# Kernel tuning notes

Hardware: AMD Instinct MI355X
Metric: run time of the kernel (lower is better)

## Reference

```python
import jax, jax.numpy as jnp
import numpy as np

N = 100000      # num nodes
E = 1600000     # num edges (avg degree ~16)
D_IN = 64
D_OUT = 64
T = 5.27        # terminal time t
K = 2           # propagation steps


def setup_inputs() -> dict:
    key = jax.random.key(0)
    k1, k2, k3 = jax.random.split(key, 3)
    x = jax.random.normal(k1, (N, D_IN), dtype=jnp.float32)
    edge_index = jax.random.randint(k2, (2, E), 0, N, dtype=jnp.int64)
    # glorot-initialized linear weight [in, out] and bias
    limit = np.sqrt(6.0 / (D_IN + D_OUT)).astype(np.float32)
    W = jax.random.uniform(k3, (D_IN, D_OUT), dtype=jnp.float32, minval=-limit, maxval=limit)
    b = jnp.zeros((D_OUT,), dtype=jnp.float32)
    return {"x": x, "edge_index": edge_index, "W": W, "b": b}


def reference(x, edge_index, W, b):
    n = x.shape[0]
    src, dst = edge_index[0], edge_index[1]
    # add self-loops
    loop = jnp.arange(n, dtype=src.dtype)
    src = jnp.concatenate([src, loop])
    dst = jnp.concatenate([dst, loop])
    w = jnp.ones((src.shape[0],), dtype=x.dtype)
    # symmetric GCN normalization: D^{-1/2} A D^{-1/2}
    deg = jax.ops.segment_sum(w, dst, num_segments=n)
    dinv = jnp.where(deg > 0, jax.lax.rsqrt(deg), jnp.zeros_like(deg))
    w = dinv[src] * w * dinv[dst]
    delta = T / K  # decoupled diffusion step size
    for _ in range(K):
        # spmm: out[i] = sum_{(j->i) in E} w_e * x[j]
        out = jax.ops.segment_sum(x[src] * w[:, None], dst, num_segments=n)
        x = (1.0 - delta) * x + delta * out
    return x @ W + b
```

## Files before the change

### kernel.cpp

```cpp
#include <hip/hip_runtime.h>
#include <hip/hip_fp16.h>


#define TPB 256
#define SCAN_T 256
#define SCAN_I 4
#define SCAN_CHUNK (SCAN_T * SCAN_I)
#define BATCH 16

__global__ void count_kernel(const int* __restrict__ dst, int* __restrict__ counts, int e) {
    int i = blockIdx.x * blockDim.x + threadIdx.x;
    if (i < e) atomicAdd(&counts[dst[i]], 1);
}

__global__ void scan_partials(const int* __restrict__ counts, int* __restrict__ bsums, int n) {
    __shared__ int red[SCAN_T];
    int t = threadIdx.x;
    int base = blockIdx.x * SCAN_CHUNK + t * SCAN_I;
    int s = 0;
#pragma unroll
    for (int k = 0; k < SCAN_I; ++k) { int i = base + k; if (i < n) s += counts[i]; }
    red[t] = s;
    __syncthreads();
    for (int off = SCAN_T / 2; off > 0; off >>= 1) {
        if (t < off) red[t] += red[t + off];
        __syncthreads();
    }
    if (t == 0) bsums[blockIdx.x] = red[0];
}

__global__ void scan_bsums(int* __restrict__ bsums, int nb, int* __restrict__ row_ptr,
                           int n, int e) {
    __shared__ int s[512];
    int t = threadIdx.x;
    int v = (t < nb) ? bsums[t] : 0;
    s[t] = v;
    __syncthreads();
    for (int off = 1; off < 512; off <<= 1) {
        int a = (t >= off) ? s[t - off] : 0;
        __syncthreads();
        s[t] += a;
        __syncthreads();
    }
    if (t < nb) bsums[t] = s[t] - v;
    if (t == 0) row_ptr[n] = e;
}

__global__ void scan_emit(const int* __restrict__ counts, const int* __restrict__ boffs,
                          int* __restrict__ row_ptr, int* __restrict__ cursor,
                          float* __restrict__ dinv, int n) {
    __shared__ int red[SCAN_T];
    int t = threadIdx.x;
    int base = blockIdx.x * SCAN_CHUNK + t * SCAN_I;
    int c[SCAN_I];
    int s = 0;
#pragma unroll
    for (int k = 0; k < SCAN_I; ++k) { int i = base + k; c[k] = (i < n) ? counts[i] : 0; s += c[k]; }
    red[t] = s;
    __syncthreads();
    for (int off = 1; off < SCAN_T; off <<= 1) {
        int a = (t >= off) ? red[t - off] : 0;
        __syncthreads();
        red[t] += a;
        __syncthreads();
    }
    int run = boffs[blockIdx.x] + red[t] - s;
#pragma unroll
    for (int k = 0; k < SCAN_I; ++k) {
        int i = base + k;
        if (i < n) {
            row_ptr[i] = run;
            cursor[i]  = run;
            dinv[i] = rsqrtf((float)(c[k] + 1));
            run += c[k];
        }
    }
}

__global__ void cast_z(const float* __restrict__ x, const float* __restrict__ dinv,
                       __half* __restrict__ zh, __half* __restrict__ z1h, int n) {
    int i = blockIdx.x * blockDim.x + threadIdx.x;
    int total = n * 64;
    if (i < total) {
        zh[i] = __float2half(dinv[i >> 6] * x[i]);
    } else if (i < total + 64) {
        zh[i]  = __float2half(0.f);
        z1h[i] = __float2half(0.f);
    }
}

__global__ void fill_kernel(const int* __restrict__ src, const int* __restrict__ dst,
                            int* __restrict__ cursor, int* __restrict__ col, int e) {
    int i = blockIdx.x * blockDim.x + threadIdx.x;
    if (i >= e) return;
    int pos = atomicAdd(&cursor[dst[i]], 1);
    col[pos] = src[i];
}

__device__ __forceinline__ float spmm_row(const __half* __restrict__ zh,
                                          const int* __restrict__ col,
                                          int beg, int end, int lane, int nzero) {
    float acc = 0.f;
    for (int j = beg; j < end; j += BATCH) {
        int c[BATCH];
#pragma unroll
        for (int k = 0; k < BATCH; ++k) {
            int jj = j + k;
            int cc = col[min(jj, end - 1)];
            c[k] = (jj < end) ? cc : nzero;
        }
        float xv[BATCH];
#pragma unroll
        for (int k = 0; k < BATCH; ++k)
            xv[k] = __half2float(zh[(unsigned)c[k] * 64u + (unsigned)lane]);
#pragma unroll
        for (int k = 0; k < BATCH; ++k) acc += xv[k];
    }
    return acc;
}

__global__ void spmm1_kernel(const float* __restrict__ x, const __half* __restrict__ zh,
                             __half* __restrict__ x1h, __half* __restrict__ z1h,
                             const int* __restrict__ row_ptr, const int* __restrict__ col,
                             const float* __restrict__ dinv, int n, float delta) {
    int node = blockIdx.x * (blockDim.x >> 6) + (threadIdx.x >> 6);
    int lane = threadIdx.x & 63;
    if (node >= n) return;
    unsigned idx = (unsigned)node * 64u + (unsigned)lane;
    float xi = x[idx];
    float dv = dinv[node];
    float acc = spmm_row(zh, col, row_ptr[node], row_ptr[node + 1], lane, n);
    float x1 = (1.f - delta) * xi + delta * dv * (dv * xi + acc);
    x1h[idx] = __float2half(x1);
    z1h[idx] = __float2half(dv * x1);
}

__global__ void spmm2_gemm_kernel(const __half* __restrict__ x1h, const __half* __restrict__ z1h,
                                  float* __restrict__ y,
                                  const int* __restrict__ row_ptr, const int* __restrict__ col,
                                  const float* __restrict__ dinv,
                                  const float* __restrict__ W, const float* __restrict__ b,
                                  int n, float delta) {
    __shared__ float Ws[64 * 64];
    __shared__ float bs[64];
    for (int i = threadIdx.x; i < 64 * 64; i += blockDim.x) Ws[i] = W[i];
    if (threadIdx.x < 64) bs[threadIdx.x] = b[threadIdx.x];
    __syncthreads();
    int node = blockIdx.x * (blockDim.x >> 6) + (threadIdx.x >> 6);
    int lane = threadIdx.x & 63;
    if (node >= n) return;
    unsigned idx = (unsigned)node * 64u + (unsigned)lane;
    float xi = __half2float(x1h[idx]);
    float dv = dinv[node];
    float acc = spmm_row(z1h, col, row_ptr[node], row_ptr[node + 1], lane, n);
    float res = (1.f - delta) * xi + delta * dv * (dv * xi + acc);
    float o = bs[lane];
#pragma unroll
    for (int k = 0; k < 64; ++k) {
        o += __shfl(res, k) * Ws[k * 64 + lane];
    }
    y[idx] = o;
}

extern "C" void kernel_launch(void* const* d_in, const int* in_sizes, int n_in,
                              void* d_out, int out_size, void* d_ws, size_t ws_size,
                              hipStream_t stream) {
    const float* x  = (const float*)d_in[0];
    const int*   ei = (const int*)d_in[1];
    const float* W  = (const float*)d_in[2];
    const float* b  = (const float*)d_in[3];
    float* out = (float*)d_out;

    const int N = in_sizes[0] / 64;
    const int E = in_sizes[1] / 2;
    const float delta = (float)(5.27 / 2.0);

    char* p = (char*)d_ws;
    __half* zh   = (__half*)p;  p += (size_t)(N + 1) * 64 * sizeof(__half);
    __half* z1h  = (__half*)p;  p += (size_t)(N + 1) * 64 * sizeof(__half);
    __half* x1h  = (__half*)p;  p += (size_t)N * 64 * sizeof(__half);
    int*   col   = (int*)p;     p += (size_t)E * sizeof(int);
    float* dinv  = (float*)p;   p += (size_t)N * sizeof(float);
    int*   counts= (int*)p;     p += (size_t)N * sizeof(int);
    int*   rowp  = (int*)p;     p += (size_t)(N + 4) * sizeof(int);
    int*   cursor= (int*)p;     p += (size_t)N * sizeof(int);
    int*   bsums = (int*)p;     p += 512 * sizeof(int);

    hipMemsetAsync(counts, 0, (size_t)N * sizeof(int), stream);

    int grid_e = (E + TPB - 1) / TPB;
    int grid_n = (N + (TPB / 64) - 1) / (TPB / 64);
    int nb_scan = (N + SCAN_CHUNK - 1) / SCAN_CHUNK;
    int grid_c = ((N + 1) * 64 + TPB - 1) / TPB;

    count_kernel<<<grid_e, TPB, 0, stream>>>(ei + E, counts, E);
    scan_partials<<<nb_scan, SCAN_T, 0, stream>>>(counts, bsums, N);
    scan_bsums<<<1, 512, 0, stream>>>(bsums, nb_scan, rowp, N, E);
    scan_emit<<<nb_scan, SCAN_T, 0, stream>>>(counts, bsums, rowp, cursor, dinv, N);
    cast_z<<<grid_c, TPB, 0, stream>>>(x, dinv, zh, z1h, N);
    fill_kernel<<<grid_e, TPB, 0, stream>>>(ei, ei + E, cursor, col, E);

    spmm1_kernel<<<grid_n, TPB, 0, stream>>>(x, zh, x1h, z1h, rowp, col, dinv, N, delta);
    spmm2_gemm_kernel<<<grid_n, TPB, 0, stream>>>(x1h, z1h, out, rowp, col, dinv, W, b, N, delta);
}
```

Baseline: 390.8 us.

## Split wave across two edges with half2 gathers, drop x1h buffer via sqrt-degree recovery

```diff
diff --git a/kernel.cpp b/kernel.cpp
--- a/kernel.cpp
+++ b/kernel.cpp
@@ -48,7 +48,7 @@
 
 __global__ void scan_emit(const int* __restrict__ counts, const int* __restrict__ boffs,
                           int* __restrict__ row_ptr, int* __restrict__ cursor,
-                          float* __restrict__ dinv, int n) {
+                          float* __restrict__ dinv, float* __restrict__ rdeg, int n) {
     __shared__ int red[SCAN_T];
     int t = threadIdx.x;
     int base = blockIdx.x * SCAN_CHUNK + t * SCAN_I;
@@ -71,7 +71,9 @@
         if (i < n) {
             row_ptr[i] = run;
             cursor[i]  = run;
-            dinv[i] = rsqrtf((float)(c[k] + 1));
+            float d = (float)(c[k] + 1);
+            dinv[i] = rsqrtf(d);
+            rdeg[i] = sqrtf(d);
             run += c[k];
         }
     }
@@ -80,12 +82,21 @@
 __global__ void cast_z(const float* __restrict__ x, const float* __restrict__ dinv,
                        __half* __restrict__ zh, __half* __restrict__ z1h, int n) {
     int i = blockIdx.x * blockDim.x + threadIdx.x;
-    int total = n * 64;
+    int total = n * 16;
     if (i < total) {
-        zh[i] = __float2half(dinv[i >> 6] * x[i]);
-    } else if (i < total + 64) {
-        zh[i]  = __float2half(0.f);
-        z1h[i] = __float2half(0.f);
+        float4 v = reinterpret_cast<const float4*>(x)[i];
+        float dv = dinv[i >> 4];
+        __half2 a, b2;
+        a.x  = __float2half(v.x * dv); a.y  = __float2half(v.y * dv);
+        b2.x = __float2half(v.z * dv); b2.y = __float2half(v.w * dv);
+        reinterpret_cast<__half2*>(zh)[2 * i]     = a;
+        reinterpret_cast<__half2*>(zh)[2 * i + 1] = b2;
+    } else if (i < total + 16) {
+        __half2 z; z.x = __float2half(0.f); z.y = __float2half(0.f);
+        reinterpret_cast<__half2*>(zh)[2 * i]      = z;
+        reinterpret_cast<__half2*>(zh)[2 * i + 1]  = z;
+        reinterpret_cast<__half2*>(z1h)[2 * i]     = z;
+        reinterpret_cast<__half2*>(z1h)[2 * i + 1] = z;
     }
 }
 
@@ -97,48 +108,56 @@
     col[pos] = src[i];
 }
 
-__device__ __forceinline__ float spmm_row(const __half* __restrict__ zh,
-                                          const int* __restrict__ col,
-                                          int beg, int end, int lane, int nzero) {
-    float acc = 0.f;
-    for (int j = beg; j < end; j += BATCH) {
+__device__ __forceinline__ float2 spmm_row2(const __half* __restrict__ zh,
+                                            const int* __restrict__ col,
+                                            int beg, int end, int sub, int m, int nzero) {
+    float a0 = 0.f, a1 = 0.f;
+    for (int j = beg; j < end; j += 2 * BATCH) {
         int c[BATCH];
 #pragma unroll
         for (int k = 0; k < BATCH; ++k) {
-            int jj = j + k;
-            int cc = col[min(jj, end - 1)];
-            c[k] = (jj < end) ? cc : nzero;
+            int e = j + 2 * k + sub;
+            int cc = col[min(e, end - 1)];
+            c[k] = (e < end) ? cc : nzero;
         }
-        float xv[BATCH];
+        __half2 v[BATCH];
 #pragma unroll
         for (int k = 0; k < BATCH; ++k)
-            xv[k] = __half2float(zh[(unsigned)c[k] * 64u + (unsigned)lane]);
-#pragma unroll
-        for (int k = 0; k < BATCH; ++k) acc += xv[k];
-    }
-    return acc;
-}
-
-__global__ void spmm1_kernel(const float* __restrict__ x, const __half* __restrict__ zh,
-                             __half* __restrict__ x1h, __half* __restrict__ z1h,
+            v[k] = *reinterpret_cast<const __half2*>(zh + (size_t)(unsigned)c[k] * 64u + 2u * (unsigned)m);
+#pragma unroll
+        for (int k = 0; k < BATCH; ++k) {
+            float2 f = __half22float2(v[k]);
+            a0 += f.x; a1 += f.y;
+        }
+    }
+    a0 += __shfl_xor(a0, 32);
+    a1 += __shfl_xor(a1, 32);
+    return make_float2(a0, a1);
+}
+
+__global__ void spmm1_kernel(const __half* __restrict__ zh, __half* __restrict__ z1h,
                              const int* __restrict__ row_ptr, const int* __restrict__ col,
-                             const float* __restrict__ dinv, int n, float delta) {
+                             const float* __restrict__ dinv, const float* __restrict__ rdeg,
+                             int n, float delta) {
     int node = blockIdx.x * (blockDim.x >> 6) + (threadIdx.x >> 6);
     int lane = threadIdx.x & 63;
     if (node >= n) return;
-    unsigned idx = (unsigned)node * 64u + (unsigned)lane;
-    float xi = x[idx];
-    float dv = dinv[node];
-    float acc = spmm_row(zh, col, row_ptr[node], row_ptr[node + 1], lane, n);
-    float x1 = (1.f - delta) * xi + delta * dv * (dv * xi + acc);
-    x1h[idx] = __float2half(x1);
-    z1h[idx] = __float2half(dv * x1);
-}
-
-__global__ void spmm2_gemm_kernel(const __half* __restrict__ x1h, const __half* __restrict__ z1h,
-                                  float* __restrict__ y,
+    int sub = lane >> 5, m = lane & 31;
+    float dv = dinv[node], rd = rdeg[node];
+    float2 acc = spmm_row2(zh, col, row_ptr[node], row_ptr[node + 1], sub, m, n);
+    __half2 zp = *reinterpret_cast<const __half2*>(zh + (size_t)node * 64 + 2 * m);
+    float2 zf = __half22float2(zp);
+    float x1x = (1.f - delta) * (zf.x * rd) + delta * dv * (zf.x + acc.x);
+    float x1y = (1.f - delta) * (zf.y * rd) + delta * dv * (zf.y + acc.y);
+    if (sub == 0) {
+        __half2 o; o.x = __float2half(dv * x1x); o.y = __float2half(dv * x1y);
+        *reinterpret_cast<__half2*>(z1h + (size_t)node * 64 + 2 * m) = o;
+    }
+}
+
+__global__ void spmm2_gemm_kernel(const __half* __restrict__ z1h, float* __restrict__ y,
                                   const int* __restrict__ row_ptr, const int* __restrict__ col,
-                                  const float* __restrict__ dinv,
+                                  const float* __restrict__ dinv, const float* __restrict__ rdeg,
                                   const float* __restrict__ W, const float* __restrict__ b,
                                   int n, float delta) {
     __shared__ float Ws[64 * 64];
@@ -149,17 +168,26 @@
     int node = blockIdx.x * (blockDim.x >> 6) + (threadIdx.x >> 6);
     int lane = threadIdx.x & 63;
     if (node >= n) return;
-    unsigned idx = (unsigned)node * 64u + (unsigned)lane;
-    float xi = __half2float(x1h[idx]);
-    float dv = dinv[node];
-    float acc = spmm_row(z1h, col, row_ptr[node], row_ptr[node + 1], lane, n);
-    float res = (1.f - delta) * xi + delta * dv * (dv * xi + acc);
-    float o = bs[lane];
-#pragma unroll
-    for (int k = 0; k < 64; ++k) {
-        o += __shfl(res, k) * Ws[k * 64 + lane];
-    }
-    y[idx] = o;
+    int sub = lane >> 5, m = lane & 31;
+    float dv = dinv[node], rd = rdeg[node];
+    float2 acc = spmm_row2(z1h, col, row_ptr[node], row_ptr[node + 1], sub, m, n);
+    __half2 zp = *reinterpret_cast<const __half2*>(z1h + (size_t)node * 64 + 2 * m);
+    float2 zf = __half22float2(zp);
+    float rx = (1.f - delta) * (zf.x * rd) + delta * dv * (zf.x + acc.x);
+    float ry = (1.f - delta) * (zf.y * rd) + delta * dv * (zf.y + acc.y);
+    float o0 = bs[2 * m], o1 = bs[2 * m + 1];
+#pragma unroll
+    for (int q = 0; q < 32; ++q) {
+        float ax = __shfl(rx, q);
+        float ay = __shfl(ry, q);
+        o0 = fmaf(ax, Ws[(2 * q) * 64 + 2 * m], o0);
+        o0 = fmaf(ay, Ws[(2 * q + 1) * 64 + 2 * m], o0);
+        o1 = fmaf(ax, Ws[(2 * q) * 64 + 2 * m + 1], o1);
+        o1 = fmaf(ay, Ws[(2 * q + 1) * 64 + 2 * m + 1], o1);
+    }
+    if (sub == 0) {
+        *reinterpret_cast<float2*>(y + (size_t)node * 64 + 2 * m) = make_float2(o0, o1);
+    }
 }
 
 extern "C" void kernel_launch(void* const* d_in, const int* in_sizes, int n_in,
@@ -178,9 +206,9 @@
     char* p = (char*)d_ws;
     __half* zh   = (__half*)p;  p += (size_t)(N + 1) * 64 * sizeof(__half);
     __half* z1h  = (__half*)p;  p += (size_t)(N + 1) * 64 * sizeof(__half);
-    __half* x1h  = (__half*)p;  p += (size_t)N * 64 * sizeof(__half);
-    int*   col   = (int*)p;     p += (size_t)E * sizeof(int);
+    int*   col   = (int*)p;     p += ((size_t)E + 64) * sizeof(int);
     float* dinv  = (float*)p;   p += (size_t)N * sizeof(float);
+    float* rdeg  = (float*)p;   p += (size_t)N * sizeof(float);
     int*   counts= (int*)p;     p += (size_t)N * sizeof(int);
     int*   rowp  = (int*)p;     p += (size_t)(N + 4) * sizeof(int);
     int*   cursor= (int*)p;     p += (size_t)N * sizeof(int);
@@ -191,15 +219,15 @@
     int grid_e = (E + TPB - 1) / TPB;
     int grid_n = (N + (TPB / 64) - 1) / (TPB / 64);
     int nb_scan = (N + SCAN_CHUNK - 1) / SCAN_CHUNK;
-    int grid_c = ((N + 1) * 64 + TPB - 1) / TPB;
+    int grid_c = (N * 16 + 16 + TPB - 1) / TPB;
 
     count_kernel<<<grid_e, TPB, 0, stream>>>(ei + E, counts, E);
     scan_partials<<<nb_scan, SCAN_T, 0, stream>>>(counts, bsums, N);
     scan_bsums<<<1, 512, 0, stream>>>(bsums, nb_scan, rowp, N, E);
-    scan_emit<<<nb_scan, SCAN_T, 0, stream>>>(counts, bsums, rowp, cursor, dinv, N);
+    scan_emit<<<nb_scan, SCAN_T, 0, stream>>>(counts, bsums, rowp, cursor, dinv, rdeg, N);
     cast_z<<<grid_c, TPB, 0, stream>>>(x, dinv, zh, z1h, N);
     fill_kernel<<<grid_e, TPB, 0, stream>>>(ei, ei + E, cursor, col, E);
 
-    spmm1_kernel<<<grid_n, TPB, 0, stream>>>(x, zh, x1h, z1h, rowp, col, dinv, N, delta);
-    spmm2_gemm_kernel<<<grid_n, TPB, 0, stream>>>(x1h, z1h, out, rowp, col, dinv, W, b, N, delta);
-}
+    spmm1_kernel<<<grid_n, TPB, 0, stream>>>(zh, z1h, rowp, col, dinv, rdeg, N, delta);
+    spmm2_gemm_kernel<<<grid_n, TPB, 0, stream>>>(z1h, out, rowp, col, dinv, rdeg, W, b, N, delta);
+}
```

Result: slower. 467.0 us (+19.5%).
